# Kernel tuning notes

Hardware: AMD Instinct MI355X
Metric: run time of the kernel (lower is better)

Reference implementation:

```python
import jax, jax.numpy as jnp
import numpy as np
from jax import lax

B_, K_, T_, V_ = 2, 4, 1024, 1024
D_MODEL, EXPAND = 512, 2
D_INNER = EXPAND * D_MODEL          # 1024
N_STATE, D_CONV, DT_RANK, L_ = 16, 4, 32, 2


def setup_inputs() -> dict:
    key = jax.random.key(0)
    ks = jax.random.split(key, 9)
    s = 0.02
    A0 = jnp.log(jnp.arange(1, N_STATE + 1, dtype=jnp.float32))  # S4D-real init
    return {
        'codes': jax.random.randint(ks[0], (B_, K_, T_), 0, V_),
        'embed_w': jax.random.normal(ks[1], (K_, V_, D_MODEL), jnp.float32) * s,
        'norm_w': jnp.ones((L_, D_MODEL), jnp.float32),
        'in_proj_w': jax.random.normal(ks[2], (L_, 2 * D_INNER, D_MODEL), jnp.float32) * s,
        'conv_w': jax.random.normal(ks[3], (L_, D_INNER, 1, D_CONV), jnp.float32) * s,
        'conv_b': jnp.zeros((L_, D_INNER), jnp.float32),
        'x_proj_w': jax.random.normal(ks[4], (L_, DT_RANK + 2 * N_STATE, D_INNER), jnp.float32) * s,
        'dt_proj_w': jax.random.normal(ks[5], (L_, D_INNER, DT_RANK), jnp.float32) * s,
        'dt_proj_b': jnp.zeros((L_, D_INNER), jnp.float32),
        'A_log': jnp.broadcast_to(A0, (L_, D_INNER, N_STATE)) + 0.0,
        'D_skip': jnp.ones((L_, D_INNER), jnp.float32),
        'out_proj_w': jax.random.normal(ks[6], (L_, D_MODEL, D_INNER), jnp.float32) * s,
        'head_w': jax.random.normal(ks[7], (K_, D_MODEL, V_), jnp.float32) * s,
    }


def rmsnorm(x, w, eps=1e-6):
    return x * w * lax.rsqrt(jnp.mean(x * x, axis=-1, keepdims=True) + eps)


def causal_dwconv(x, w, b):
    # x: (B,T,D); w: (D,1,d_conv) depthwise; torch pads d_conv-1 both sides then slices [:T]
    # == left-pad-only causal conv.
    xt = x.transpose(0, 2, 1)  # (B,D,T)
    y = lax.conv_general_dilated(xt, w, (1,), [(D_CONV - 1, 0)],
                                 feature_group_count=D_INNER,
                                 dimension_numbers=('NCH', 'OIH', 'NCH'))
    return (y + b[None, :, None]).transpose(0, 2, 1)


def mamba_block(x, norm_w, in_w, cw, cb, xp_w, dtp_w, dtp_b, A_log, D_skip, out_w):
    res = x
    x = rmsnorm(x, norm_w)
    xz = x @ in_w.T                                   # (B,T,2*d_inner)
    x_ssm, z = jnp.split(xz, 2, axis=-1)
    x_ssm = jax.nn.silu(causal_dwconv(x_ssm, cw, cb))  # (B,T,D)
    x_dbl = x_ssm @ xp_w.T                            # (B,T,dt_rank+2N)
    dt_lr, Bm, Cm = jnp.split(x_dbl, [DT_RANK, DT_RANK + N_STATE], axis=-1)
    dt = jax.nn.softplus(dt_lr @ dtp_w.T + dtp_b)     # (B,T,D)
    A = -jnp.exp(A_log)                               # (D,N)
    dA = jnp.exp(dt[..., None] * A)                   # (B,T,D,N)
    dBx = dt[..., None] * Bm[:, :, None, :] * x_ssm[..., None]  # (B,T,D,N)

    def step(h, inp):
        dA_t, dBx_t, C_t = inp
        h = dA_t * h + dBx_t                          # (B,D,N)
        return h, jnp.einsum('bdn,bn->bd', h, C_t)

    h0 = jnp.zeros((x.shape[0], D_INNER, N_STATE), x.dtype)
    _, ys = lax.scan(step, h0, (dA.transpose(1, 0, 2, 3),
                                dBx.transpose(1, 0, 2, 3),
                                Cm.transpose(1, 0, 2)))
    y = ys.transpose(1, 0, 2) + x_ssm * D_skip        # (B,T,D)
    y = y * jax.nn.silu(z)
    return res + y @ out_w.T


def reference(codes, embed_w, norm_w, in_proj_w, conv_w, conv_b, x_proj_w,
              dt_proj_w, dt_proj_b, A_log, D_skip, out_proj_w, head_w):
    k_idx = jnp.arange(K_)[None, :, None]
    x = embed_w[k_idx, codes].sum(axis=1)             # (B,T,d_model): RVQ sum-embedding
    for l in range(L_):
        x = mamba_block(x, norm_w[l], in_proj_w[l], conv_w[l], conv_b[l],
                        x_proj_w[l], dt_proj_w[l], dt_proj_b[l],
                        A_log[l], D_skip[l], out_proj_w[l])
    return jnp.einsum('btd,kdv->bktv', x, head_w)     # (B,K,T,V)
```

## Files before the change

kernel.cpp:

```cpp
#include <hip/hip_runtime.h>
#include <hip/hip_bf16.h>


#define B_SZ 2
#define K_CB 4
#define T_SZ 1024
#define V_SZ 1024
#define DM 512
#define DI 1024
#define NS 16
#define DTR 32
#define NCHUNK 64
#define TCHUNK 16

typedef unsigned short u16;
typedef long long ll;
using short8 = __attribute__((ext_vector_type(8))) short;
using f32x4  = __attribute__((ext_vector_type(4))) float;

__device__ __forceinline__ float bf2f(u16 u) {
    union { unsigned int i; float f; } v; v.i = ((unsigned int)u) << 16; return v.f;
}
__device__ __forceinline__ u16 f2bf(float f) {
    union { float f; unsigned int i; } v; v.f = f;
    unsigned int x = v.i;
    return (u16)((x + 0x7fffu + ((x >> 16) & 1u)) >> 16);
}
__device__ __forceinline__ float siluf(float x) { return x / (1.f + __expf(-x)); }
__device__ __forceinline__ float softplusf(float x) { return (x > 20.f) ? x : log1pf(__expf(x)); }

__global__ __launch_bounds__(256) void mega0_k(const float* __restrict__ in_w,
                                               const float* __restrict__ xp_w,
                                               const float* __restrict__ dtp_w,
                                               const float* __restrict__ out_w,
                                               u16* __restrict__ w_in, u16* __restrict__ w_xp,
                                               u16* __restrict__ w_dt, u16* __restrict__ w_out,
                                               const float* __restrict__ head_w,
                                               u16* __restrict__ w_hd,
                                               const int* __restrict__ codes,
                                               const float* __restrict__ ew,
                                               const float* __restrict__ nw,
                                               float* __restrict__ x,
                                               u16* __restrict__ xn) {
    __shared__ float tile[64][65];
    int bid = blockIdx.x;
    int tid = threadIdx.x;
    if (bid < 3264) {
        int i = (bid * 256 + tid) << 2;
        const float* s; u16* d;
        if (i < 2097152) { s = in_w + i; d = w_in + i; }
        else {
            i -= 2097152;
            if (i < 131072) { s = xp_w + i; d = w_xp + i; }
            else {
                i -= 131072;
                if (i < 65536) { s = dtp_w + i; d = w_dt + i; }
                else { i -= 65536; s = out_w + i; d = w_out + i; }
            }
        }
        float4 v = *(const float4*)s;
        ushort4 o; o.x = f2bf(v.x); o.y = f2bf(v.y); o.z = f2bf(v.z); o.w = f2bf(v.w);
        *(ushort4*)d = o;
    } else if (bid < 3776) {
        int idx = bid - 3264;
        int z = idx >> 7, rest = idx & 127;
        int d0 = (rest >> 4) << 6, v0 = (rest & 15) << 6;
        int col = tid & 63, rbase = tid >> 6;
#pragma unroll
        for (int i = 0; i < 16; i++) {
            int row = (i << 2) + rbase;
            tile[row][col] = head_w[(ll)z * (DM * V_SZ) + (ll)(d0 + row) * V_SZ + v0 + col];
        }
        __syncthreads();
#pragma unroll
        for (int i = 0; i < 16; i++) {
            int vrow = (i << 2) + rbase;
            w_hd[(ll)z * (V_SZ * DM) + (ll)(v0 + vrow) * DM + d0 + col] = f2bf(tile[col][vrow]);
        }
    } else {
        int row = bid - 3776;
        int b = row >> 10, t = row & 1023;
        float a0 = 0.f, a1 = 0.f;
#pragma unroll
        for (int k = 0; k < K_CB; k++) {
            int c = codes[b * (K_CB * T_SZ) + k * T_SZ + t];
            a0 += ew[((ll)k * V_SZ + c) * DM + tid];
            a1 += ew[((ll)k * V_SZ + c) * DM + tid + 256];
        }
        x[(ll)row * DM + tid]       = a0;
        x[(ll)row * DM + tid + 256] = a1;
        float ss = a0 * a0 + a1 * a1;
#pragma unroll
        for (int off = 32; off > 0; off >>= 1) ss += __shfl_down(ss, off, 64);
        float* red = &tile[0][0];
        if ((tid & 63) == 0) red[tid >> 6] = ss;
        __syncthreads();
        float tot = red[0] + red[1] + red[2] + red[3];
        float scale = rsqrtf(tot * (1.0f / DM) + 1e-6f);
        xn[(ll)row * DM + tid]       = f2bf(a0 * scale * nw[tid]);
        xn[(ll)row * DM + tid + 256] = f2bf(a1 * scale * nw[tid + 256]);
    }
}

__global__ __launch_bounds__(256) void rmsnorm_k(const float* __restrict__ x,
                                                 const float* __restrict__ w,
                                                 u16* __restrict__ xn) {
    ll row = blockIdx.x;
    const float* xr = x + row * DM;
    int tid = threadIdx.x;
    float v0 = xr[tid], v1 = xr[tid + 256];
    float ss = v0 * v0 + v1 * v1;
#pragma unroll
    for (int off = 32; off > 0; off >>= 1) ss += __shfl_down(ss, off, 64);
    __shared__ float red[4];
    if ((tid & 63) == 0) red[tid >> 6] = ss;
    __syncthreads();
    float tot = red[0] + red[1] + red[2] + red[3];
    float scale = rsqrtf(tot * (1.0f / DM) + 1e-6f);
    xn[row * DM + tid]       = f2bf(v0 * scale * w[tid]);
    xn[row * DM + tid + 256] = f2bf(v1 * scale * w[tid + 256]);
}

template <int EP>
__global__ __launch_bounds__(256) void mgemm2_k(const u16* __restrict__ A, int lda,
                                                const u16* __restrict__ W,
                                                float* __restrict__ C,
                                                u16* __restrict__ Cb, int ldcb, int K) {
    __shared__ u16 As[2][4096];
    __shared__ u16 Bs[2][4096];
    int tid = threadIdx.x;
    int wave = tid >> 6, lane = tid & 63;
    int q = lane >> 4, r = lane & 15;
    int m0 = blockIdx.y << 7, n0 = blockIdx.x << 7;
    int wm = (wave >> 1) << 6, wn = (wave & 1) << 6;
    int srow = tid >> 1, soff = (tid & 1) << 4;
    const u16* Ap = A + (ll)(m0 + srow) * lda + soff;
    const u16* Wp = W + (ll)(n0 + srow) * K + soff;
    int sidx = (srow << 5) + soff;
    f32x4 acc[4][4];
#pragma unroll
    for (int i = 0; i < 4; i++)
#pragma unroll
        for (int j = 0; j < 4; j++) acc[i][j] = (f32x4){0.f, 0.f, 0.f, 0.f};

    uint4 ra0 = *(const uint4*)Ap,       ra1 = *(const uint4*)(Ap + 8);
    uint4 rb0 = *(const uint4*)Wp,       rb1 = *(const uint4*)(Wp + 8);
    *(uint4*)&As[0][sidx] = ra0; *(uint4*)&As[0][sidx + 8] = ra1;
    *(uint4*)&Bs[0][sidx] = rb0; *(uint4*)&Bs[0][sidx + 8] = rb1;
    __syncthreads();

    int p = 0;
    for (int k0 = 0; k0 < K; k0 += 32) {
        bool pf = (k0 + 32) < K;
        if (pf) {
            ra0 = *(const uint4*)(Ap + k0 + 32); ra1 = *(const uint4*)(Ap + k0 + 40);
            rb0 = *(const uint4*)(Wp + k0 + 32); rb1 = *(const uint4*)(Wp + k0 + 40);
        }
        short8 af[4], bfr[4];
#pragma unroll
        for (int i = 0; i < 4; i++) af[i]  = *(const short8*)&As[p][((wm + (i << 4) + r) << 5) + (q << 3)];
#pragma unroll
        for (int j = 0; j < 4; j++) bfr[j] = *(const short8*)&Bs[p][((wn + (j << 4) + r) << 5) + (q << 3)];
#pragma unroll
        for (int i = 0; i < 4; i++)
#pragma unroll
            for (int j = 0; j < 4; j++)
                acc[i][j] = __builtin_amdgcn_mfma_f32_16x16x32_bf16(af[i], bfr[j], acc[i][j], 0, 0, 0);
        if (pf) {
            *(uint4*)&As[p ^ 1][sidx] = ra0; *(uint4*)&As[p ^ 1][sidx + 8] = ra1;
            *(uint4*)&Bs[p ^ 1][sidx] = rb0; *(uint4*)&Bs[p ^ 1][sidx + 8] = rb1;
        }
        __syncthreads();
        p ^= 1;
    }

#pragma unroll
    for (int i = 0; i < 4; i++)
#pragma unroll
        for (int j = 0; j < 4; j++)
#pragma unroll
            for (int g = 0; g < 4; g++) {
                int m = m0 + wm + (i << 4) + (q << 2) + g;
                int n = n0 + wn + (j << 4) + r;
                float v = acc[i][j][g];
                if (EP == 0) {
                    Cb[(ll)m * ldcb + n] = f2bf(v);
                } else {
                    int z = n >> 10, vv = n & 1023;
                    int b = m >> 10, t = m & 1023;
                    C[((ll)(b * K_CB + z) * T_SZ + t) * V_SZ + vv] = v;
                }
            }
}

template <int EP>
__global__ __launch_bounds__(256) void mgemm_k(const u16* __restrict__ A, int lda,
                                               const u16* __restrict__ W,
                                               float* __restrict__ C, int ldc, int K,
                                               const float* __restrict__ bias,
                                               u16* __restrict__ Cb, int ldcb) {
    __shared__ u16 As[2][2048];
    __shared__ u16 Bs[2][2048];
    int tid = threadIdx.x;
    int m0 = blockIdx.y << 6, n0 = blockIdx.x << 6;
    int lane = tid & 63, wave = tid >> 6;
    int q = lane >> 4, r = lane & 15;
    int wm = (wave >> 1) << 5, wn = (wave & 1) << 5;
    int srow = tid >> 2, soff = (tid & 3) << 3;
    const u16* Ap = A + (ll)(m0 + srow) * lda + soff;
    const u16* Wp = W + (ll)(n0 + srow) * K + soff;
    int sidx = (srow << 5) + soff;
    f32x4 acc[2][2];
#pragma unroll
    for (int i = 0; i < 2; i++)
#pragma unroll
        for (int j = 0; j < 2; j++) acc[i][j] = (f32x4){0.f, 0.f, 0.f, 0.f};

    uint4 ra = *(const uint4*)Ap;
    uint4 rb = *(const uint4*)Wp;
    *(uint4*)&As[0][sidx] = ra;
    *(uint4*)&Bs[0][sidx] = rb;
    __syncthreads();

    int p = 0;
    for (int k0 = 0; k0 < K; k0 += 32) {
        bool pf = (k0 + 32) < K;
        if (pf) {
            ra = *(const uint4*)(Ap + k0 + 32);
            rb = *(const uint4*)(Wp + k0 + 32);
        }
        short8 af[2], bfr[2];
#pragma unroll
        for (int i = 0; i < 2; i++) af[i]  = *(const short8*)&As[p][((wm + (i << 4) + r) << 5) + (q << 3)];
#pragma unroll
        for (int j = 0; j < 2; j++) bfr[j] = *(const short8*)&Bs[p][((wn + (j << 4) + r) << 5) + (q << 3)];
#pragma unroll
        for (int i = 0; i < 2; i++)
#pragma unroll
            for (int j = 0; j < 2; j++)
                acc[i][j] = __builtin_amdgcn_mfma_f32_16x16x32_bf16(af[i], bfr[j], acc[i][j], 0, 0, 0);
        if (pf) {
            *(uint4*)&As[p ^ 1][sidx] = ra;
            *(uint4*)&Bs[p ^ 1][sidx] = rb;
        }
        __syncthreads();
        p ^= 1;
    }

#pragma unroll
    for (int i = 0; i < 2; i++)
#pragma unroll
        for (int j = 0; j < 2; j++)
#pragma unroll
            for (int g = 0; g < 4; g++) {
                int m = m0 + wm + (i << 4) + (q << 2) + g;
                int n = n0 + wn + (j << 4) + r;
                float v = acc[i][j][g];
                if (EP == 1) {
                    C[(ll)m * ldc + n] = v;
                    Cb[(ll)m * ldcb + n] = f2bf(v);
                } else if (EP == 2) {
                    C[(ll)m * ldc + n] = softplusf(v + bias[n]);
                } else {
                    float nv = C[(ll)m * ldc + n] + v;
                    C[(ll)m * ldc + n] = nv;
                    Cb[(ll)m * ldcb + n] = f2bf(nv);
                }
            }
}

__global__ __launch_bounds__(256) void conv_k(const u16* __restrict__ xzb,
                                              const float* __restrict__ cw,
                                              const float* __restrict__ cb,
                                              float* __restrict__ xc,
                                              u16* __restrict__ xcb) {
    int row = blockIdx.x;
    int b = row >> 10, t = row & 1023;
    int c0 = threadIdx.x << 2;
    float4 a = *(const float4*)&cb[c0];
    float acc[4] = {a.x, a.y, a.z, a.w};
    float4 cwv[4];
#pragma unroll
    for (int e = 0; e < 4; e++) cwv[e] = *(const float4*)&cw[(c0 + e) << 2];
#pragma unroll
    for (int j = 0; j < 4; j++) {
        int tt = t - 3 + j;
        if (tt >= 0) {
            ushort4 v = *(const ushort4*)&xzb[((ll)(b * T_SZ + tt)) * (2 * DI) + c0];
            acc[0] = fmaf(bf2f(v.x), ((const float*)&cwv[0])[j], acc[0]);
            acc[1] = fmaf(bf2f(v.y), ((const float*)&cwv[1])[j], acc[1]);
            acc[2] = fmaf(bf2f(v.z), ((const float*)&cwv[2])[j], acc[2]);
            acc[3] = fmaf(bf2f(v.w), ((const float*)&cwv[3])[j], acc[3]);
        }
    }
    float4 s; ushort4 sb;
    s.x = siluf(acc[0]); s.y = siluf(acc[1]); s.z = siluf(acc[2]); s.w = siluf(acc[3]);
    sb.x = f2bf(s.x); sb.y = f2bf(s.y); sb.z = f2bf(s.z); sb.w = f2bf(s.w);
    *(float4*)&xc[(ll)row * DI + c0] = s;
    *(ushort4*)&xcb[(ll)row * DI + c0] = sb;
}

__global__ __launch_bounds__(256) void scan1_k(const float* __restrict__ dt,
                                               const float* __restrict__ xc,
                                               const float* __restrict__ xdbl,
                                               const float* __restrict__ A_log,
                                               float* __restrict__ pA, float* __restrict__ U) {
    int blk = blockIdx.x;
    int dblk = blk & 3;
    int c = (blk >> 2) & (NCHUNK - 1);
    int b = blk >> 8;
    int d = dblk * 256 + threadIdx.x;
    int t0 = c * TCHUNK;
    __shared__ float BC[TCHUNK][32];
    if (threadIdx.x < TCHUNK * 8) {
        int rr = threadIdx.x >> 3, cc = (threadIdx.x & 7) << 2;
        *(float4*)&BC[rr][cc] = *(const float4*)&xdbl[((ll)(b * T_SZ + t0 + rr)) * 64 + DTR + cc];
    }
    float Av[NS];
#pragma unroll
    for (int n4 = 0; n4 < 4; n4++) {
        float4 alv = *(const float4*)&A_log[d * NS + (n4 << 2)];
        Av[(n4 << 2) + 0] = -__expf(alv.x); Av[(n4 << 2) + 1] = -__expf(alv.y);
        Av[(n4 << 2) + 2] = -__expf(alv.z); Av[(n4 << 2) + 3] = -__expf(alv.w);
    }
    __syncthreads();
    float p[NS], u[NS];
#pragma unroll
    for (int n = 0; n < NS; n++) { p[n] = 1.f; u[n] = 0.f; }
#pragma unroll
    for (int s = 0; s < TCHUNK; s++) {
        ll ro = (ll)(b * T_SZ + t0 + s);
        float dtv = dt[ro * DI + d];
        float xv = xc[ro * DI + d];
        float dx = dtv * xv;
#pragma unroll
        for (int n = 0; n < NS; n++) {
            float aa = __expf(dtv * Av[n]);
            p[n] *= aa;
            u[n] = fmaf(aa, u[n], dx * BC[s][n]);
        }
    }
    ll o = (((ll)b * NCHUNK + c) * DI + d) * NS;
#pragma unroll
    for (int n = 0; n < NS; n++) { pA[o + n] = p[n]; U[o + n] = u[n]; }
}

__global__ __launch_bounds__(256) void scan2_k(const float* __restrict__ pA,
                                               const float* __restrict__ U,
                                               float* __restrict__ hst) {
    int i = blockIdx.x * 256 + threadIdx.x;
    int b = i >> 14;
    int rest = i & 16383;
    float h = 0.f;
#pragma unroll
    for (int c = 0; c < NCHUNK; c++) {
        ll o = ((ll)b * NCHUNK + c) * (DI * NS) + rest;
        float pa = pA[o], u = U[o];
        hst[o] = h;
        h = fmaf(pa, h, u);
    }
}

__global__ __launch_bounds__(256) void scan3_k(const float* __restrict__ dt,
                                               const float* __restrict__ xc,
                                               const float* __restrict__ xdbl,
                                               const u16* __restrict__ xzb,
                                               const float* __restrict__ A_log,
                                               const float* __restrict__ Dk,
                                               const float* __restrict__ hst,
                                               u16* __restrict__ y) {
    int blk = blockIdx.x;
    int dblk = blk & 3;
    int c = (blk >> 2) & (NCHUNK - 1);
    int b = blk >> 8;
    int d = dblk * 256 + threadIdx.x;
    int t0 = c * TCHUNK;
    __shared__ float BC[TCHUNK][32];
    if (threadIdx.x < TCHUNK * 8) {
        int rr = threadIdx.x >> 3, cc = (threadIdx.x & 7) << 2;
        *(float4*)&BC[rr][cc] = *(const float4*)&xdbl[((ll)(b * T_SZ + t0 + rr)) * 64 + DTR + cc];
    }
    float Av[NS];
#pragma unroll
    for (int n4 = 0; n4 < 4; n4++) {
        float4 alv = *(const float4*)&A_log[d * NS + (n4 << 2)];
        Av[(n4 << 2) + 0] = -__expf(alv.x); Av[(n4 << 2) + 1] = -__expf(alv.y);
        Av[(n4 << 2) + 2] = -__expf(alv.z); Av[(n4 << 2) + 3] = -__expf(alv.w);
    }
    float h[NS];
    ll ho = (((ll)b * NCHUNK + c) * DI + d) * NS;
#pragma unroll
    for (int n = 0; n < NS; n++) h[n] = hst[ho + n];
    float Dv = Dk[d];
    __syncthreads();
#pragma unroll
    for (int s = 0; s < TCHUNK; s++) {
        ll ro = (ll)(b * T_SZ + t0 + s);
        float dtv = dt[ro * DI + d];
        float xv = xc[ro * DI + d];
        float dx = dtv * xv;
        float acc = 0.f;
#pragma unroll
        for (int n = 0; n < NS; n++) {
            float aa = __expf(dtv * Av[n]);
            h[n] = fmaf(aa, h[n], dx * BC[s][n]);
            acc = fmaf(h[n], BC[s][16 + n], acc);
        }
        float zv = bf2f(xzb[ro * (2 * DI) + DI + d]);
        y[ro * DI + d] = f2bf((acc + xv * Dv) * siluf(zv));
    }
}

extern "C" void kernel_launch(void* const* d_in, const int* in_sizes, int n_in,
                              void* d_out, int out_size, void* d_ws, size_t ws_size,
                              hipStream_t stream) {
    const int*   codes   = (const int*)d_in[0];
    const float* embed_w = (const float*)d_in[1];
    const float* norm_w  = (const float*)d_in[2];
    const float* in_w    = (const float*)d_in[3];
    const float* conv_w  = (const float*)d_in[4];
    const float* conv_b  = (const float*)d_in[5];
    const float* xp_w    = (const float*)d_in[6];
    const float* dtp_w   = (const float*)d_in[7];
    const float* dtp_b   = (const float*)d_in[8];
    const float* A_log   = (const float*)d_in[9];
    const float* D_skip  = (const float*)d_in[10];
    const float* out_w   = (const float*)d_in[11];
    const float* head_w  = (const float*)d_in[12];
    float* out = (float*)d_out;

    float* ws = (float*)d_ws;
    float* x    = ws;
    float* xc   = x + 1048576;
    float* dtb  = xc + 2097152;
    float* xdbl = dtb + 2097152;
    float* pA   = xdbl + 131072;
    float* Uh   = pA + 2097152;

    u16* us       = (u16*)(Uh + 2097152);
    u16* xz_bf    = us;
    u16* xc_bf    = xz_bf + 4194304;
    u16* ybxn_bf  = xc_bf + 2097152;
    u16* xdbl_bf  = ybxn_bf + 2097152;
    u16* w_in_bf  = xdbl_bf + 131072;
    u16* w_xp_bf  = w_in_bf + 2097152;
    u16* w_dt_bf  = w_xp_bf + 131072;
    u16* w_out_bf = w_dt_bf + 65536;
    u16* w_hd_bf  = w_out_bf + 1048576;

    u16* xn_bf = ybxn_bf;
    u16* y_bf  = ybxn_bf;
    u16* x_bf  = xc_bf;

    mega0_k<<<5824, 256, 0, stream>>>(in_w, xp_w, dtp_w, out_w,
                                      w_in_bf, w_xp_bf, w_dt_bf, w_out_bf,
                                      head_w, w_hd_bf, codes, embed_w, norm_w, x, xn_bf);

    for (int l = 0; l < 2; l++) {
        const float* al = A_log + l * DI * NS;
        if (l == 1)
            rmsnorm_k<<<2048, 256, 0, stream>>>(x, norm_w + DM, xn_bf);
        mgemm2_k<0><<<dim3(16, 16), 256, 0, stream>>>(xn_bf, DM, w_in_bf + l * 1048576,
                                                      nullptr, xz_bf, 2 * DI, DM);
        conv_k<<<2048, 256, 0, stream>>>(xz_bf, conv_w + l * DI * 4, conv_b + l * DI, xc, xc_bf);
        mgemm_k<1><<<dim3(1, 32), 256, 0, stream>>>(xc_bf, DI, w_xp_bf + l * 65536,
                                                    xdbl, 64, DI, nullptr, xdbl_bf, 64);
        mgemm_k<2><<<dim3(16, 32), 256, 0, stream>>>(xdbl_bf, 64, w_dt_bf + l * 32768,
                                                     dtb, DI, DTR, dtp_b + l * DI, nullptr, 0);
        scan1_k<<<512, 256, 0, stream>>>(dtb, xc, xdbl, al, pA, Uh);
        scan2_k<<<128, 256, 0, stream>>>(pA, Uh, Uh);
        scan3_k<<<512, 256, 0, stream>>>(dtb, xc, xdbl, xz_bf, al, D_skip + l * DI, Uh, y_bf);
        mgemm_k<3><<<dim3(8, 32), 256, 0, stream>>>(y_bf, DI, w_out_bf + l * 524288,
                                                    x, DM, DI, nullptr, x_bf, DM);
    }

    mgemm2_k<4><<<dim3(32, 16), 256, 0, stream>>>(x_bf, DM, w_hd_bf, out, nullptr, 0, DM);
}
```

Before: 309.8 us.

## Fuse dt projection and softplus into scan kernels, dropping dt GEMM

Removes the separate dt_proj GEMM (with its softplus epilogue) and the fp32 dt buffer. Both scan kernels now load each channel's 32 dt_proj weights and bias into registers and recompute dt per timestep from the x_dbl row held in shared memory. This saves one launch plus the write and two reads of a 2M-float dt tensor per layer. In exchange, the 32-FMA dot product and the softplus are computed twice (in scan1 and scan3), register pressure rises, and dt is now computed in fp32 instead of from bf16 operands.

```diff
diff --git a/kernel.cpp b/kernel.cpp
--- a/kernel.cpp
+++ b/kernel.cpp
@@ -31,10 +31,9 @@
 
 __global__ __launch_bounds__(256) void mega0_k(const float* __restrict__ in_w,
                                                const float* __restrict__ xp_w,
-                                               const float* __restrict__ dtp_w,
                                                const float* __restrict__ out_w,
                                                u16* __restrict__ w_in, u16* __restrict__ w_xp,
-                                               u16* __restrict__ w_dt, u16* __restrict__ w_out,
+                                               u16* __restrict__ w_out,
                                                const float* __restrict__ head_w,
                                                u16* __restrict__ w_hd,
                                                const int* __restrict__ codes,
@@ -45,24 +44,20 @@
     __shared__ float tile[64][65];
     int bid = blockIdx.x;
     int tid = threadIdx.x;
-    if (bid < 3264) {
+    if (bid < 3200) {
         int i = (bid * 256 + tid) << 2;
         const float* s; u16* d;
         if (i < 2097152) { s = in_w + i; d = w_in + i; }
         else {
             i -= 2097152;
             if (i < 131072) { s = xp_w + i; d = w_xp + i; }
-            else {
-                i -= 131072;
-                if (i < 65536) { s = dtp_w + i; d = w_dt + i; }
-                else { i -= 65536; s = out_w + i; d = w_out + i; }
-            }
+            else { i -= 131072; s = out_w + i; d = w_out + i; }
         }
         float4 v = *(const float4*)s;
         ushort4 o; o.x = f2bf(v.x); o.y = f2bf(v.y); o.z = f2bf(v.z); o.w = f2bf(v.w);
         *(ushort4*)d = o;
-    } else if (bid < 3776) {
-        int idx = bid - 3264;
+    } else if (bid < 3712) {
+        int idx = bid - 3200;
         int z = idx >> 7, rest = idx & 127;
         int d0 = (rest >> 4) << 6, v0 = (rest & 15) << 6;
         int col = tid & 63, rbase = tid >> 6;
@@ -78,7 +73,7 @@
             w_hd[(ll)z * (V_SZ * DM) + (ll)(v0 + vrow) * DM + d0 + col] = f2bf(tile[col][vrow]);
         }
     } else {
-        int row = bid - 3776;
+        int row = bid - 3712;
         int b = row >> 10, t = row & 1023;
         float a0 = 0.f, a1 = 0.f;
 #pragma unroll
@@ -258,9 +253,6 @@
                 float v = acc[i][j][g];
                 if (EP == 1) {
                     C[(ll)m * ldc + n] = v;
-                    Cb[(ll)m * ldcb + n] = f2bf(v);
-                } else if (EP == 2) {
-                    C[(ll)m * ldc + n] = softplusf(v + bias[n]);
                 } else {
                     float nv = C[(ll)m * ldc + n] + v;
                     C[(ll)m * ldc + n] = nv;
@@ -300,21 +292,22 @@
     *(ushort4*)&xcb[(ll)row * DI + c0] = sb;
 }
 
-__global__ __launch_bounds__(256) void scan1_k(const float* __restrict__ dt,
-                                               const float* __restrict__ xc,
+__global__ __launch_bounds__(256) void scan1_k(const float* __restrict__ xc,
                                                const float* __restrict__ xdbl,
                                                const float* __restrict__ A_log,
+                                               const float* __restrict__ wdt,
+                                               const float* __restrict__ bdt,
                                                float* __restrict__ pA, float* __restrict__ U) {
-    int blk = blockIdx.x;
+    int blk = blockIdx.x, tid = threadIdx.x;
     int dblk = blk & 3;
     int c = (blk >> 2) & (NCHUNK - 1);
     int b = blk >> 8;
-    int d = dblk * 256 + threadIdx.x;
+    int d = dblk * 256 + tid;
     int t0 = c * TCHUNK;
-    __shared__ float BC[TCHUNK][32];
-    if (threadIdx.x < TCHUNK * 8) {
-        int rr = threadIdx.x >> 3, cc = (threadIdx.x & 7) << 2;
-        *(float4*)&BC[rr][cc] = *(const float4*)&xdbl[((ll)(b * T_SZ + t0 + rr)) * 64 + DTR + cc];
+    __shared__ float BC[TCHUNK][64];
+    {
+        int rr = tid >> 4, cc = (tid & 15) << 2;
+        *(float4*)&BC[rr][cc] = *(const float4*)&xdbl[((ll)(b * T_SZ + t0 + rr)) * 64 + cc];
     }
     float Av[NS];
 #pragma unroll
@@ -323,6 +316,14 @@
         Av[(n4 << 2) + 0] = -__expf(alv.x); Av[(n4 << 2) + 1] = -__expf(alv.y);
         Av[(n4 << 2) + 2] = -__expf(alv.z); Av[(n4 << 2) + 3] = -__expf(alv.w);
     }
+    float wr[DTR];
+#pragma unroll
+    for (int k4 = 0; k4 < 8; k4++) {
+        float4 wv = *(const float4*)&wdt[(ll)d * DTR + (k4 << 2)];
+        wr[(k4 << 2) + 0] = wv.x; wr[(k4 << 2) + 1] = wv.y;
+        wr[(k4 << 2) + 2] = wv.z; wr[(k4 << 2) + 3] = wv.w;
+    }
+    float bias = bdt[d];
     __syncthreads();
     float p[NS], u[NS];
 #pragma unroll
@@ -330,14 +331,17 @@
 #pragma unroll
     for (int s = 0; s < TCHUNK; s++) {
         ll ro = (ll)(b * T_SZ + t0 + s);
-        float dtv = dt[ro * DI + d];
-        float xv = xc[ro * DI + d];
-        float dx = dtv * xv;
+        float acc = bias;
+#pragma unroll
+        for (int k = 0; k < DTR; k++) acc = fmaf(BC[s][k], wr[k], acc);
+        float dtl = softplusf(acc);
+        float xl = xc[ro * DI + d];
+        float dx = dtl * xl;
 #pragma unroll
         for (int n = 0; n < NS; n++) {
-            float aa = __expf(dtv * Av[n]);
+            float aa = __expf(dtl * Av[n]);
             p[n] *= aa;
-            u[n] = fmaf(aa, u[n], dx * BC[s][n]);
+            u[n] = fmaf(aa, u[n], dx * BC[s][32 + n]);
         }
     }
     ll o = (((ll)b * NCHUNK + c) * DI + d) * NS;
@@ -361,24 +365,25 @@
     }
 }
 
-__global__ __launch_bounds__(256) void scan3_k(const float* __restrict__ dt,
-                                               const float* __restrict__ xc,
+__global__ __launch_bounds__(256) void scan3_k(const float* __restrict__ xc,
                                                const float* __restrict__ xdbl,
                                                const u16* __restrict__ xzb,
                                                const float* __restrict__ A_log,
+                                               const float* __restrict__ wdt,
+                                               const float* __restrict__ bdt,
                                                const float* __restrict__ Dk,
                                                const float* __restrict__ hst,
                                                u16* __restrict__ y) {
-    int blk = blockIdx.x;
+    int blk = blockIdx.x, tid = threadIdx.x;
     int dblk = blk & 3;
     int c = (blk >> 2) & (NCHUNK - 1);
     int b = blk >> 8;
-    int d = dblk * 256 + threadIdx.x;
+    int d = dblk * 256 + tid;
     int t0 = c * TCHUNK;
-    __shared__ float BC[TCHUNK][32];
-    if (threadIdx.x < TCHUNK * 8) {
-        int rr = threadIdx.x >> 3, cc = (threadIdx.x & 7) << 2;
-        *(float4*)&BC[rr][cc] = *(const float4*)&xdbl[((ll)(b * T_SZ + t0 + rr)) * 64 + DTR + cc];
+    __shared__ float BC[TCHUNK][64];
+    {
+        int rr = tid >> 4, cc = (tid & 15) << 2;
+        *(float4*)&BC[rr][cc] = *(const float4*)&xdbl[((ll)(b * T_SZ + t0 + rr)) * 64 + cc];
     }
     float Av[NS];
 #pragma unroll
@@ -387,6 +392,14 @@
         Av[(n4 << 2) + 0] = -__expf(alv.x); Av[(n4 << 2) + 1] = -__expf(alv.y);
         Av[(n4 << 2) + 2] = -__expf(alv.z); Av[(n4 << 2) + 3] = -__expf(alv.w);
     }
+    float wr[DTR];
+#pragma unroll
+    for (int k4 = 0; k4 < 8; k4++) {
+        float4 wv = *(const float4*)&wdt[(ll)d * DTR + (k4 << 2)];
+        wr[(k4 << 2) + 0] = wv.x; wr[(k4 << 2) + 1] = wv.y;
+        wr[(k4 << 2) + 2] = wv.z; wr[(k4 << 2) + 3] = wv.w;
+    }
+    float bias = bdt[d];
     float h[NS];
     ll ho = (((ll)b * NCHUNK + c) * DI + d) * NS;
 #pragma unroll
@@ -396,18 +409,21 @@
 #pragma unroll
     for (int s = 0; s < TCHUNK; s++) {
         ll ro = (ll)(b * T_SZ + t0 + s);
-        float dtv = dt[ro * DI + d];
-        float xv = xc[ro * DI + d];
-        float dx = dtv * xv;
-        float acc = 0.f;
+        float acc = bias;
+#pragma unroll
+        for (int k = 0; k < DTR; k++) acc = fmaf(BC[s][k], wr[k], acc);
+        float dtl = softplusf(acc);
+        float xl = xc[ro * DI + d];
+        float dx = dtl * xl;
+        float oacc = 0.f;
 #pragma unroll
         for (int n = 0; n < NS; n++) {
-            float aa = __expf(dtv * Av[n]);
-            h[n] = fmaf(aa, h[n], dx * BC[s][n]);
-            acc = fmaf(h[n], BC[s][16 + n], acc);
+            float aa = __expf(dtl * Av[n]);
+            h[n] = fmaf(aa, h[n], dx * BC[s][32 + n]);
+            oacc = fmaf(h[n], BC[s][48 + n], oacc);
         }
         float zv = bf2f(xzb[ro * (2 * DI) + DI + d]);
-        y[ro * DI + d] = f2bf((acc + xv * Dv) * siluf(zv));
+        y[ro * DI + d] = f2bf((oacc + xl * Dv) * siluf(zv));
     }
 }
 
@@ -432,8 +448,7 @@
     float* ws = (float*)d_ws;
     float* x    = ws;
     float* xc   = x + 1048576;
-    float* dtb  = xc + 2097152;
-    float* xdbl = dtb + 2097152;
+    float* xdbl = xc + 2097152;
     float* pA   = xdbl + 131072;
     float* Uh   = pA + 2097152;
 
@@ -441,35 +456,34 @@
     u16* xz_bf    = us;
     u16* xc_bf    = xz_bf + 4194304;
     u16* ybxn_bf  = xc_bf + 2097152;
-    u16* xdbl_bf  = ybxn_bf + 2097152;
-    u16* w_in_bf  = xdbl_bf + 131072;
+    u16* w_in_bf  = ybxn_bf + 2097152;
     u16* w_xp_bf  = w_in_bf + 2097152;
-    u16* w_dt_bf  = w_xp_bf + 131072;
-    u16* w_out_bf = w_dt_bf + 65536;
+    u16* w_out_bf = w_xp_bf + 131072;
     u16* w_hd_bf  = w_out_bf + 1048576;
 
     u16* xn_bf = ybxn_bf;
     u16* y_bf  = ybxn_bf;
     u16* x_bf  = xc_bf;
 
-    mega0_k<<<5824, 256, 0, stream>>>(in_w, xp_w, dtp_w, out_w,
-                                      w_in_bf, w_xp_bf, w_dt_bf, w_out_bf,
+    mega0_k<<<5760, 256, 0, stream>>>(in_w, xp_w, out_w,
+                                      w_in_bf, w_xp_bf, w_out_bf,
                                       head_w, w_hd_bf, codes, embed_w, norm_w, x, xn_bf);
 
     for (int l = 0; l < 2; l++) {
-        const float* al = A_log + l * DI * NS;
+        const float* al   = A_log + l * DI * NS;
+        const float* wdtl = dtp_w + (ll)l * DI * DTR;
+        const float* bdtl = dtp_b + l * DI;
+        const float* Dkl  = D_skip + l * DI;
         if (l == 1)
             rmsnorm_k<<<2048, 256, 0, stream>>>(x, norm_w + DM, xn_bf);
         mgemm2_k<0><<<dim3(16, 16), 256, 0, stream>>>(xn_bf, DM, w_in_bf + l * 1048576,
                                                       nullptr, xz_bf, 2 * DI, DM);
         conv_k<<<2048, 256, 0, stream>>>(xz_bf, conv_w + l * DI * 4, conv_b + l * DI, xc, xc_bf);
         mgemm_k<1><<<dim3(1, 32), 256, 0, stream>>>(xc_bf, DI, w_xp_bf + l * 65536,
-                                                    xdbl, 64, DI, nullptr, xdbl_bf, 64);
-        mgemm_k<2><<<dim3(16, 32), 256, 0, stream>>>(xdbl_bf, 64, w_dt_bf + l * 32768,
-                                                     dtb, DI, DTR, dtp_b + l * DI, nullptr, 0);
-        scan1_k<<<512, 256, 0, stream>>>(dtb, xc, xdbl, al, pA, Uh);
+                                                    xdbl, 64, DI, nullptr, nullptr, 0);
+        scan1_k<<<512, 256, 0, stream>>>(xc, xdbl, al, wdtl, bdtl, pA, Uh);
         scan2_k<<<128, 256, 0, stream>>>(pA, Uh, Uh);
-        scan3_k<<<512, 256, 0, stream>>>(dtb, xc, xdbl, xz_bf, al, D_skip + l * DI, Uh, y_bf);
+        scan3_k<<<512, 256, 0, stream>>>(xc, xdbl, xz_bf, al, wdtl, bdtl, Dkl, Uh, y_bf);
         mgemm_k<3><<<dim3(8, 32), 256, 0, stream>>>(y_bf, DI, w_out_bf + l * 524288,
                                                     x, DM, DI, nullptr, x_bf, DM);
     }
```

After: 341.3 us. +10.2%, slower.

## Fuse dt projection GEMM with softplus into first chunked scan pass

Applied to the files above, without the earlier changes.

Merges the dt_proj GEMM (with bias and softplus) and the scan1 chunk-local pass into one kernel. Each block computes a 64x64 dt tile with MFMA, keeps it in shared memory, and runs the 16-step chunk recurrence for 4 chunks by 64 channels. This removes one launch and the read-back of dt from global memory in scan1. dt is still written to global for scan3, and the work per block is regrouped, giving 64-thread-wide channel groups instead of 256.

```diff
diff --git a/kernel.cpp b/kernel.cpp
--- a/kernel.cpp
+++ b/kernel.cpp
@@ -259,8 +259,6 @@
                 if (EP == 1) {
                     C[(ll)m * ldc + n] = v;
                     Cb[(ll)m * ldcb + n] = f2bf(v);
-                } else if (EP == 2) {
-                    C[(ll)m * ldc + n] = softplusf(v + bias[n]);
                 } else {
                     float nv = C[(ll)m * ldc + n] + v;
                     C[(ll)m * ldc + n] = nv;
@@ -300,47 +298,93 @@
     *(ushort4*)&xcb[(ll)row * DI + c0] = sb;
 }
 
-__global__ __launch_bounds__(256) void scan1_k(const float* __restrict__ dt,
-                                               const float* __restrict__ xc,
-                                               const float* __restrict__ xdbl,
-                                               const float* __restrict__ A_log,
-                                               float* __restrict__ pA, float* __restrict__ U) {
-    int blk = blockIdx.x;
-    int dblk = blk & 3;
-    int c = (blk >> 2) & (NCHUNK - 1);
-    int b = blk >> 8;
-    int d = dblk * 256 + threadIdx.x;
-    int t0 = c * TCHUNK;
-    __shared__ float BC[TCHUNK][32];
-    if (threadIdx.x < TCHUNK * 8) {
-        int rr = threadIdx.x >> 3, cc = (threadIdx.x & 7) << 2;
-        *(float4*)&BC[rr][cc] = *(const float4*)&xdbl[((ll)(b * T_SZ + t0 + rr)) * 64 + DTR + cc];
-    }
+__global__ __launch_bounds__(256) void dtscan1_k(const u16* __restrict__ A,
+                                                 const u16* __restrict__ W,
+                                                 const float* __restrict__ bias,
+                                                 const float* __restrict__ xc,
+                                                 const float* __restrict__ xdbl,
+                                                 const float* __restrict__ A_log,
+                                                 float* __restrict__ dtb,
+                                                 float* __restrict__ pA,
+                                                 float* __restrict__ U) {
+    __shared__ u16 As[2048];
+    __shared__ u16 Bs[2048];
+    __shared__ float dts[64][65];
+    __shared__ float BCs[64][16];
+    int tid = threadIdx.x;
+    int m0 = blockIdx.y << 6, n0 = blockIdx.x << 6;
+    int lane = tid & 63, wave = tid >> 6;
+    int q = lane >> 4, r = lane & 15;
+    int wm = (wave >> 1) << 5, wn = (wave & 1) << 5;
+    {
+        int srow = tid >> 2, soff = (tid & 3) << 3;
+        *(uint4*)&As[(srow << 5) + soff] = *(const uint4*)(A + (ll)(m0 + srow) * 64 + soff);
+        *(uint4*)&Bs[(srow << 5) + soff] = *(const uint4*)(W + (ll)(n0 + srow) * DTR + soff);
+        int rr = tid >> 2, cc = (tid & 3) << 2;
+        *(float4*)&BCs[rr][cc] = *(const float4*)&xdbl[(ll)(m0 + rr) * 64 + DTR + cc];
+    }
+    int sd = lane;
+    int sc = wave;
+    int dg = n0 + sd;
     float Av[NS];
 #pragma unroll
     for (int n4 = 0; n4 < 4; n4++) {
-        float4 alv = *(const float4*)&A_log[d * NS + (n4 << 2)];
+        float4 alv = *(const float4*)&A_log[dg * NS + (n4 << 2)];
         Av[(n4 << 2) + 0] = -__expf(alv.x); Av[(n4 << 2) + 1] = -__expf(alv.y);
         Av[(n4 << 2) + 2] = -__expf(alv.z); Av[(n4 << 2) + 3] = -__expf(alv.w);
     }
     __syncthreads();
+
+    f32x4 acc[2][2];
+#pragma unroll
+    for (int i = 0; i < 2; i++)
+#pragma unroll
+        for (int j = 0; j < 2; j++) acc[i][j] = (f32x4){0.f, 0.f, 0.f, 0.f};
+    short8 af[2], bfr[2];
+#pragma unroll
+    for (int i = 0; i < 2; i++) af[i]  = *(const short8*)&As[((wm + (i << 4) + r) << 5) + (q << 3)];
+#pragma unroll
+    for (int j = 0; j < 2; j++) bfr[j] = *(const short8*)&Bs[((wn + (j << 4) + r) << 5) + (q << 3)];
+#pragma unroll
+    for (int i = 0; i < 2; i++)
+#pragma unroll
+        for (int j = 0; j < 2; j++)
+            acc[i][j] = __builtin_amdgcn_mfma_f32_16x16x32_bf16(af[i], bfr[j], acc[i][j], 0, 0, 0);
+
+#pragma unroll
+    for (int i = 0; i < 2; i++)
+#pragma unroll
+        for (int j = 0; j < 2; j++)
+#pragma unroll
+            for (int g = 0; g < 4; g++) {
+                int mm = wm + (i << 4) + (q << 2) + g;
+                int nn = wn + (j << 4) + r;
+                float dtl = softplusf(acc[i][j][g] + bias[n0 + nn]);
+                dtb[(ll)(m0 + mm) * DI + (n0 + nn)] = dtl;
+                dts[mm][nn] = dtl;
+            }
+    __syncthreads();
+
+    int b = m0 >> 10;
+    int c = ((m0 & 1023) >> 4) + sc;
+    int tl0 = sc << 4;
     float p[NS], u[NS];
 #pragma unroll
     for (int n = 0; n < NS; n++) { p[n] = 1.f; u[n] = 0.f; }
 #pragma unroll
     for (int s = 0; s < TCHUNK; s++) {
-        ll ro = (ll)(b * T_SZ + t0 + s);
-        float dtv = dt[ro * DI + d];
-        float xv = xc[ro * DI + d];
+        int tl = tl0 + s;
+        float dtv = dts[tl][sd];
+        float xv = xc[(ll)(m0 + tl) * DI + dg];
         float dx = dtv * xv;
 #pragma unroll
         for (int n = 0; n < NS; n++) {
             float aa = __expf(dtv * Av[n]);
             p[n] *= aa;
-            u[n] = fmaf(aa, u[n], dx * BC[s][n]);
-        }
-    }
-    ll o = (((ll)b * NCHUNK + c) * DI + d) * NS;
+            u[n] = fmaf(aa, u[n], dx * BCs[tl][n]);
+        }
+    }
+    ll o = (((ll)b * NCHUNK + c) * DI + dg) * NS;
 #pragma unroll
     for (int n = 0; n < NS; n++) { pA[o + n] = p[n]; U[o + n] = u[n]; }
 }
@@ -465,9 +509,9 @@
         conv_k<<<2048, 256, 0, stream>>>(xz_bf, conv_w + l * DI * 4, conv_b + l * DI, xc, xc_bf);
         mgemm_k<1><<<dim3(1, 32), 256, 0, stream>>>(xc_bf, DI, w_xp_bf + l * 65536,
                                                     xdbl, 64, DI, nullptr, xdbl_bf, 64);
-        mgemm_k<2><<<dim3(16, 32), 256, 0, stream>>>(xdbl_bf, 64, w_dt_bf + l * 32768,
-                                                     dtb, DI, DTR, dtp_b + l * DI, nullptr, 0);
-        scan1_k<<<512, 256, 0, stream>>>(dtb, xc, xdbl, al, pA, Uh);
+        dtscan1_k<<<dim3(16, 32), 256, 0, stream>>>(xdbl_bf, w_dt_bf + l * 32768,
+                                                    dtp_b + l * DI, xc, xdbl, al,
+                                                    dtb, pA, Uh);
         scan2_k<<<128, 256, 0, stream>>>(pA, Uh, Uh);
         scan3_k<<<512, 256, 0, stream>>>(dtb, xc, xdbl, xz_bf, al, D_skip + l * DI, Uh, y_bf);
         mgemm_k<3><<<dim3(8, 32), 256, 0, stream>>>(y_bf, DI, w_out_bf + l * 524288,
```

Result: faster. 302.9 us (-2.2%).
